# Kernel optimization log

Measured on AMD Instinct MI355X. Metric: run time of the kernel, lower is better.

Reference implementation:

```python
import jax, jax.numpy as jnp
import numpy as np

ROPE_BASE = 10000.0
WINDOW = 1024  # per_layer_sliding_window
SCALE = 0.08838834764831845  # 1/sqrt(128)
NEG_INF = -1e30


def _apply_rope(x, positions):
    # x: [B, S, H, D]; positions: [B, S] int
    D = x.shape[-1]
    inv_freq = 1.0 / (ROPE_BASE ** (jnp.arange(0, D, 2, dtype=jnp.float32) / D))  # [D/2]
    ang = positions.astype(jnp.float32)[..., None] * inv_freq          # [B, S, D/2]
    cos = jnp.cos(ang)[:, :, None, :]                                   # [B, S, 1, D/2]
    sin = jnp.sin(ang)[:, :, None, :]
    x1, x2 = x[..., : D // 2], x[..., D // 2 :]
    return jnp.concatenate([x1 * cos - x2 * sin, x2 * cos + x1 * sin], axis=-1)


def setup_inputs() -> dict:
    key = jax.random.key(0)
    k1, k2, k3, k4 = jax.random.split(key, 4)
    B, S, H, KV, D = 1, 2048, 32, 8, 128
    q = jax.random.normal(k1, (B, S, H, D), dtype=jnp.float32)
    k = jax.random.normal(k2, (B, S, KV, D), dtype=jnp.float32)
    v = jax.random.normal(k3, (B, S, KV, D), dtype=jnp.float32)
    positions = jnp.broadcast_to(jnp.arange(S, dtype=jnp.int32), (B, S))
    sinks = jax.random.normal(k4, (H,), dtype=jnp.float32)
    return {"q": q, "k": k, "v": v, "positions": positions, "sinks": sinks}


def reference(q, k, v, positions, sinks):
    # q: [B,S,H,D]; k,v: [B,S,KV,D]; positions: [B,S]; sinks: [H]
    B, S, H, D = q.shape
    KV = k.shape[2]
    group = H // KV

    qr = _apply_rope(q, positions)
    kr = _apply_rope(k, positions)

    # GQA: expand kv heads to match q heads
    kr = jnp.repeat(kr, group, axis=2)  # [B,S,H,D]
    ve = jnp.repeat(v, group, axis=2)   # [B,S,H,D]

    scores = jnp.einsum("bqhd,bkhd->bhqk", qr, kr) * SCALE  # [B,H,Q,K]

    pq = positions[:, :, None]  # [B,Q,1]
    pk = positions[:, None, :]  # [B,1,K]
    allowed = (pk <= pq) & (pq - pk < WINDOW)               # causal + sliding window
    scores = jnp.where(allowed[:, None, :, :], scores, NEG_INF)

    # softmax with per-head attention sink logit in the denominator
    sink = sinks[None, :, None]                             # [1,H,1]
    m = jnp.maximum(jnp.max(scores, axis=-1), sink)         # [B,H,Q]
    p = jnp.exp(scores - m[..., None])                      # [B,H,Q,K]
    denom = jnp.sum(p, axis=-1) + jnp.exp(sink - m)         # [B,H,Q]
    out = jnp.einsum("bhqk,bkhd->bqhd", p, ve) / denom.transpose(0, 2, 1)[..., None]
    return out  # [B,S,H,D]
```

## Files before the change

### kernel.cpp

```cpp
#include <hip/hip_runtime.h>

#define S_LEN 2048
#define NH 32
#define NKV 8
#define HD 128
#define WINDOW 1024
#define NEG_INF_F -1e30f
#define NEG_L2_10K_O64 -0.2076205059304601f
#define LOG2E_F 1.442695040888963f

typedef unsigned short ushort_t;
typedef __attribute__((ext_vector_type(4))) short bf16x4;
typedef __attribute__((ext_vector_type(8))) short short8;
typedef __attribute__((ext_vector_type(2))) unsigned uint2v;
typedef __attribute__((ext_vector_type(4))) float floatx4;

static __device__ __forceinline__ float fexp2(float x) {
  return __builtin_amdgcn_exp2f(x);
}

static __device__ __forceinline__ ushort_t f2bf(float f) {
  union { float f; unsigned u; } un; un.f = f;
  unsigned r = un.u + 0x7fffu + ((un.u >> 16) & 1u);
  return (ushort_t)(r >> 16);
}

static __device__ __forceinline__ unsigned pack2bf(float a, float b) {
  return (unsigned)f2bf(a) | ((unsigned)f2bf(b) << 16);
}

static __device__ __forceinline__ unsigned packP(float a, float b) {
  unsigned ua = __builtin_bit_cast(unsigned, a) + 0x8000u;
  unsigned ub = __builtin_bit_cast(unsigned, b) + 0x8000u;
  return __builtin_amdgcn_perm(ub, ua, 0x07060302u);
}

__device__ __forceinline__ void gl_lds16(const ushort_t* g, ushort_t* l) {
  __builtin_amdgcn_global_load_lds(
      (const __attribute__((address_space(1))) unsigned int*)g,
      (__attribute__((address_space(3))) unsigned int*)l, 16, 0, 0);
}

__global__ __launch_bounds__(256) void prep_kv(
    const float* __restrict__ k, const float* __restrict__ v,
    const int* __restrict__ positions, ushort_t* __restrict__ Kr,
    ushort_t* __restrict__ Vt) {
  __shared__ float lv[16][129];
  const int kv = blockIdx.x & 7;
  const int s0 = (blockIdx.x >> 3) * 16;
  const int tid = threadIdx.x;
  {
    const int i = tid & 63;
    const int wrow = tid >> 6;
    const float invf = fexp2((float)i * NEG_L2_10K_O64);
#pragma unroll
    for (int it = 0; it < 4; ++it) {
      int s = s0 + it * 4 + wrow;
      float pos = (float)positions[s];
      const float* kp = k + ((size_t)s * NKV + kv) * HD;
      float x1 = kp[i], x2 = kp[i + 64];
      float sn, cs;
      __sincosf(pos * invf, &sn, &cs);
      ushort_t* o = Kr + ((size_t)kv * S_LEN + s) * HD;
      o[i] = f2bf(x1 * cs - x2 * sn);
      o[i + 64] = f2bf(x2 * cs + x1 * sn);
    }
  }
  {
    const int d = tid & 127;
    const int r2 = tid >> 7;
#pragma unroll
    for (int it = 0; it < 8; ++it) {
      int row = it * 2 + r2;
      lv[row][d] = v[((size_t)(s0 + row) * NKV + kv) * HD + d];
    }
  }
  __syncthreads();
  {
    unsigned* Vreg = (unsigned*)(Vt + ((size_t)(kv * 32 + (s0 >> 6)) * HD) * 64);
    const int jg0 = (s0 & 63) >> 1;
#pragma unroll
    for (int it = 0; it < 4; ++it) {
      int idx = it * 256 + tid;
      int d = idx >> 3, jl = idx & 7;
      Vreg[d * 32 + jg0 + jl] = pack2bf(lv[2 * jl][d], lv[2 * jl + 1][d]);
    }
  }
}

__global__ __launch_bounds__(256, 3) void attn_kernel(
    const float* __restrict__ q, const int* __restrict__ positions,
    const float* __restrict__ sinks, const ushort_t* __restrict__ Kr,
    const ushort_t* __restrict__ Vt, float* __restrict__ out) {
  __shared__ __align__(16) ushort_t smem[24576];
  __shared__ float lsx[64];

  const int tid = threadIdx.x;
  const int w = tid >> 6;
  const int lane = tid & 63;
  const int quad = lane >> 4;
  const int l16 = lane & 15;
  const int hp = w >> 1;
  const int kh = w & 1;
  const int kv = blockIdx.x & 7;
  const int bid = blockIdx.x >> 3;
  const int h0 = kv * 4 + hp * 2;
  const float QSCALE = (float)(0.08838834764831845 * 1.4426950408889634);

  const ushort_t* KrH = Kr + (size_t)kv * S_LEN * HD;
  const ushort_t* VtH = Vt + (size_t)kv * 32 * HD * 64;

  int tiles[2];
  int ntiles;
  if (bid < 64) { tiles[0] = bid + 64; tiles[1] = 0; ntiles = 1; }
  else          { tiles[0] = bid - 64; tiles[1] = 127 - bid; ntiles = 2; }

  int kgo0, kgo1, vgo0, vgo1;
  { int key = tid >> 4;          kgo0 = key * HD + (((tid & 15) ^ (key & 15)) * 8); }
  { int s2 = 256 + tid; int key = s2 >> 4;
                                 kgo1 = key * HD + (((s2 & 15) ^ (key & 15)) * 8); }
  { int n = tid;       vgo0 = (n >> 2) * 64 + (((n & 3) ^ ((n >> 4) & 3)) * 8); }
  { int n = 256 + tid; vgo1 = (n >> 2) * 64 + (((n & 3) ^ ((n >> 4) & 3)) * 8); }
  const int kdst0 = (tid & 192) * 8;
  const int kdst1 = (256 + (tid & 192)) * 8;
  const int vdst0 = (tid & 192) * 8;
  const int vdst1 = 2048 + (tid & 192) * 8;
  const int kb8 = kh * 2 + (quad >> 1);
  const int vrd = (l16 * 4 + (kb8 ^ (l16 >> 2))) * 8 + (quad & 1) * 4;
  int kro[4];
#pragma unroll
  for (int t = 0; t < 4; ++t)
    kro[t] = (kh * 16) * 128 + l16 * 128 + (((4 * t + quad) ^ l16) * 8);

  auto stage = [&](int b, int koff) {
    const ushort_t* kb = KrH + (size_t)koff * HD;
    const ushort_t* vb = VtH + (size_t)(koff >> 6) * HD * 64 + (koff & 32);
    ushort_t* Kb = smem + b * 4096;
    ushort_t* Vb = smem + 12288 + b * 4096;
    gl_lds16(kb + kgo0, Kb + kdst0);
    gl_lds16(kb + kgo1, Kb + kdst1);
    gl_lds16(vb + vgo0, Vb + vdst0);
    gl_lds16(vb + vgo1, Vb + vdst1);
  };

  for (int ti = 0; ti < ntiles; ++ti) {
    const int tile = tiles[ti];
    const int q0 = tile * 16;

    {
      const int hw = kv * 4 + w;
      ushort_t* Qsw = smem + w * 2048;
      const float invf = fexp2((float)lane * NEG_L2_10K_O64);
#pragma unroll 4
      for (int row = 0; row < 16; ++row) {
        float pos = (float)positions[q0 + row];
        const float* qp = q + ((size_t)(q0 + row) * NH + hw) * HD;
        float x1 = qp[lane], x2 = qp[lane + 64];
        float sn, cs;
        __sincosf(pos * invf, &sn, &cs);
        float o1 = (x1 * cs - x2 * sn) * QSCALE;
        float o2 = (x2 * cs + x1 * sn) * QSCALE;
        int c1_ = (lane >> 3) ^ row;
        int c2_ = ((lane >> 3) + 8) ^ row;
        Qsw[row * 128 + c1_ * 8 + (lane & 7)] = f2bf(o1);
        Qsw[row * 128 + c2_ * 8 + (lane & 7)] = f2bf(o2);
      }
    }
    __syncthreads();
    short8 qf0[4], qf1[4];
    {
      const ushort_t* Qr0 = smem + (hp * 2) * 2048;
      const ushort_t* Qr1 = smem + (hp * 2 + 1) * 2048;
#pragma unroll
      for (int t = 0; t < 4; ++t) {
        int off = l16 * 128 + (((4 * t + quad) ^ l16) * 8);
        qf0[t] = *(const short8*)&Qr0[off];
        qf1[t] = *(const short8*)&Qr1[off];
      }
    }
    __syncthreads();

    floatx4 OA[8], OB[8];
#pragma unroll
    for (int i = 0; i < 8; ++i) {
      OA[i] = (floatx4){0.f, 0.f, 0.f, 0.f};
      OB[i] = (floatx4){0.f, 0.f, 0.f, 0.f};
    }
    float lsumA = 0.f, lsumB = 0.f;

    const int cbeg = (q0 > 1023) ? ((q0 - 1023) >> 5) : 0;
    const int cend = (q0 + 15) >> 5;

    stage(0, cbeg * 32);
    if (cbeg < cend) stage(1, cbeg * 32 + 32);
    __syncthreads();

    short8 kcur[4];
#pragma unroll
    for (int t = 0; t < 4; ++t) kcur[t] = *(const short8*)&smem[kro[t]];

    int b = 0;
    for (int ci = cbeg; ci <= cend; ++ci) {
      const int koff = ci * 32;
      if (ci + 2 <= cend) {
        int bp2 = (b >= 1) ? (b - 1) : (b + 2);
        stage(bp2, koff + 64);
      }
      const int bn = (b == 2) ? 0 : b + 1;
      short8 knxt[4];
      {
        const ushort_t* KsN = smem + bn * 4096;
#pragma unroll
        for (int t = 0; t < 4; ++t) knxt[t] = *(const short8*)&KsN[kro[t]];
      }

      floatx4 sA = {0.f, 0.f, 0.f, 0.f}, sB = {0.f, 0.f, 0.f, 0.f};
#pragma unroll
      for (int t = 0; t < 4; ++t) {
        sA = __builtin_amdgcn_mfma_f32_16x16x32_bf16(kcur[t], qf0[t], sA, 0, 0, 0);
        sB = __builtin_amdgcn_mfma_f32_16x16x32_bf16(kcur[t], qf1[t], sB, 0, 0, 0);
      }

      if (koff + 31 > q0 || koff < q0 - 1008) {
        const int qp_ = q0 + l16;
        const int kb_ = koff + kh * 16 + quad * 4;
#pragma unroll
        for (int r = 0; r < 4; ++r) {
          int ki = kb_ + r;
          bool ok = (ki <= qp_) && (qp_ - ki < WINDOW);
          if (!ok) { sA[r] = NEG_INF_F; sB[r] = NEG_INF_F; }
        }
      }

      float pA[4], pB[4];
#pragma unroll
      for (int r = 0; r < 4; ++r) { pA[r] = fexp2(sA[r]); pB[r] = fexp2(sB[r]); }
      lsumA += (pA[0] + pA[1]) + (pA[2] + pA[3]);
      lsumB += (pB[0] + pB[1]) + (pB[2] + pB[3]);

      uint2v ua, ub;
      ua[0] = packP(pA[0], pA[1]); ua[1] = packP(pA[2], pA[3]);
      ub[0] = packP(pB[0], pB[1]); ub[1] = packP(pB[2], pB[3]);
      bf16x4 pfA = __builtin_bit_cast(bf16x4, ua);
      bf16x4 pfB = __builtin_bit_cast(bf16x4, ub);

      const ushort_t* VsB = smem + 12288 + b * 4096;
#pragma unroll
      for (int dt = 0; dt < 8; ++dt) {
        bf16x4 vf = *(const bf16x4*)&VsB[vrd + dt * 512];
        OA[dt] = __builtin_amdgcn_mfma_f32_16x16x16bf16_1k(vf, pfA, OA[dt], 0, 0, 0);
        OB[dt] = __builtin_amdgcn_mfma_f32_16x16x16bf16_1k(vf, pfB, OB[dt], 0, 0, 0);
      }

      __syncthreads();
#pragma unroll
      for (int t = 0; t < 4; ++t) kcur[t] = knxt[t];
      b = bn;
    }

    lsumA += __shfl_xor(lsumA, 16); lsumA += __shfl_xor(lsumA, 32);
    lsumB += __shfl_xor(lsumB, 16); lsumB += __shfl_xor(lsumB, 32);
    float* Lf = (float*)smem;
    const int lfb = lane * 4;
    float rlA = 0.f, rlB = 0.f;

    if (kh == 1 && quad == 0) {
      lsx[hp * 32 + l16] = lsumA;
      lsx[hp * 32 + 16 + l16] = lsumB;
    }
#pragma unroll
    for (int m = 0; m < 2; ++m) {
      if (kh == 1) {
#pragma unroll
        for (int t = 0; t < 4; ++t) {
          *(floatx4*)&Lf[((hp * 2 + 0) * 4 + t) * 256 + lfb] = OA[m * 4 + t];
          *(floatx4*)&Lf[((hp * 2 + 1) * 4 + t) * 256 + lfb] = OB[m * 4 + t];
        }
      }
      __syncthreads();
      if (kh == 0) {
        if (m == 0) {
          float denA = lsumA + lsx[hp * 32 + l16] + fexp2(sinks[h0] * LOG2E_F);
          float denB = lsumB + lsx[hp * 32 + 16 + l16] + fexp2(sinks[h0 + 1] * LOG2E_F);
          rlA = 1.0f / denA;
          rlB = 1.0f / denB;
        }
        float* opA = out + ((size_t)(q0 + l16) * NH + h0) * HD + quad * 4;
        float* opB = opA + HD;
#pragma unroll
        for (int t = 0; t < 4; ++t) {
          floatx4 pv = *(const floatx4*)&Lf[((hp * 2 + 0) * 4 + t) * 256 + lfb];
          floatx4 vv;
#pragma unroll
          for (int e = 0; e < 4; ++e) vv[e] = (OA[m * 4 + t][e] + pv[e]) * rlA;
          *(floatx4*)(opA + (m * 4 + t) * 16) = vv;
          pv = *(const floatx4*)&Lf[((hp * 2 + 1) * 4 + t) * 256 + lfb];
#pragma unroll
          for (int e = 0; e < 4; ++e) vv[e] = (OB[m * 4 + t][e] + pv[e]) * rlB;
          *(floatx4*)(opB + (m * 4 + t) * 16) = vv;
        }
      }
      __syncthreads();
    }
  }
}

extern "C" void kernel_launch(void* const* d_in, const int* in_sizes, int n_in,
                              void* d_out, int out_size, void* d_ws, size_t ws_size,
                              hipStream_t stream) {
  const float* q = (const float*)d_in[0];
  const float* k = (const float*)d_in[1];
  const float* v = (const float*)d_in[2];
  const int* positions = (const int*)d_in[3];
  const float* sinks = (const float*)d_in[4];
  float* out = (float*)d_out;

  ushort_t* Kr = (ushort_t*)d_ws;
  ushort_t* Vt = Kr + (size_t)NKV * S_LEN * HD;

  prep_kv<<<NKV * (S_LEN / 16), 256, 0, stream>>>(k, v, positions, Kr, Vt);
  attn_kernel<<<NKV * 96, 256, 0, stream>>>(q, positions, sinks, Kr, Vt, out);
}
```

Before: 132.8 us.

## Per-wave K staging with direct global V fragment loads, drop block barriers

```diff
diff --git a/kernel.cpp b/kernel.cpp
--- a/kernel.cpp
+++ b/kernel.cpp
@@ -77,13 +77,16 @@
   }
   __syncthreads();
   {
-    unsigned* Vreg = (unsigned*)(Vt + ((size_t)(kv * 32 + (s0 >> 6)) * HD) * 64);
+    unsigned* Vreg = (unsigned*)Vt + (size_t)kv * 131072 + (s0 >> 6) * 4096;
     const int jg0 = (s0 & 63) >> 1;
 #pragma unroll
     for (int it = 0; it < 4; ++it) {
       int idx = it * 256 + tid;
       int d = idx >> 3, jl = idx & 7;
-      Vreg[d * 32 + jg0 + jl] = pack2bf(lv[2 * jl][d], lv[2 * jl + 1][d]);
+      int jg = jg0 + jl;
+      int o = (jg >> 3) * 1024 + (d >> 4) * 128 +
+              (((jg >> 1) & 3) * 16 + (d & 15)) * 2 + (jg & 1);
+      Vreg[o] = pack2bf(lv[2 * jl][d], lv[2 * jl + 1][d]);
     }
   }
 }
@@ -92,7 +95,7 @@
     const float* __restrict__ q, const int* __restrict__ positions,
     const float* __restrict__ sinks, const ushort_t* __restrict__ Kr,
     const ushort_t* __restrict__ Vt, float* __restrict__ out) {
-  __shared__ __align__(16) ushort_t smem[24576];
+  __shared__ __align__(16) ushort_t smem[16384];
   __shared__ float lsx[64];
 
   const int tid = threadIdx.x;
@@ -108,39 +111,28 @@
   const float QSCALE = (float)(0.08838834764831845 * 1.4426950408889634);
 
   const ushort_t* KrH = Kr + (size_t)kv * S_LEN * HD;
-  const ushort_t* VtH = Vt + (size_t)kv * 32 * HD * 64;
+  const ushort_t* VtH = Vt + (size_t)kv * 262144;
 
   int tiles[2];
   int ntiles;
   if (bid < 64) { tiles[0] = bid + 64; tiles[1] = 0; ntiles = 1; }
   else          { tiles[0] = bid - 64; tiles[1] = 127 - bid; ntiles = 2; }
 
-  int kgo0, kgo1, vgo0, vgo1;
-  { int key = tid >> 4;          kgo0 = key * HD + (((tid & 15) ^ (key & 15)) * 8); }
-  { int s2 = 256 + tid; int key = s2 >> 4;
-                                 kgo1 = key * HD + (((s2 & 15) ^ (key & 15)) * 8); }
-  { int n = tid;       vgo0 = (n >> 2) * 64 + (((n & 3) ^ ((n >> 4) & 3)) * 8); }
-  { int n = 256 + tid; vgo1 = (n >> 2) * 64 + (((n & 3) ^ ((n >> 4) & 3)) * 8); }
-  const int kdst0 = (tid & 192) * 8;
-  const int kdst1 = (256 + (tid & 192)) * 8;
-  const int vdst0 = (tid & 192) * 8;
-  const int vdst1 = 2048 + (tid & 192) * 8;
-  const int kb8 = kh * 2 + (quad >> 1);
-  const int vrd = (l16 * 4 + (kb8 ^ (l16 >> 2))) * 8 + (quad & 1) * 4;
+  ushort_t* kslot = smem + w * 4096;
+
   int kro[4];
 #pragma unroll
   for (int t = 0; t < 4; ++t)
-    kro[t] = (kh * 16) * 128 + l16 * 128 + (((4 * t + quad) ^ l16) * 8);
-
-  auto stage = [&](int b, int koff) {
-    const ushort_t* kb = KrH + (size_t)koff * HD;
-    const ushort_t* vb = VtH + (size_t)(koff >> 6) * HD * 64 + (koff & 32);
-    ushort_t* Kb = smem + b * 4096;
-    ushort_t* Vb = smem + 12288 + b * 4096;
-    gl_lds16(kb + kgo0, Kb + kdst0);
-    gl_lds16(kb + kgo1, Kb + kdst1);
-    gl_lds16(vb + vgo0, Vb + vdst0);
-    gl_lds16(vb + vgo1, Vb + vdst1);
+    kro[t] = l16 * 128 + (((4 * t + quad) ^ l16) * 8);
+
+  auto wstage = [&](int buf, int koff) {
+    const ushort_t* kb = KrH + (size_t)(koff + kh * 16) * HD;
+    ushort_t* dst = kslot + buf * 2048;
+#pragma unroll
+    for (int i = 0; i < 4; ++i) {
+      int rl = i * 4 + (lane >> 4);
+      gl_lds16(kb + rl * HD + (((lane & 15) ^ rl) * 8), dst + i * 512);
+    }
   };
 
   for (int ti = 0; ti < ntiles; ++ti) {
@@ -191,27 +183,45 @@
     const int cbeg = (q0 > 1023) ? ((q0 - 1023) >> 5) : 0;
     const int cend = (q0 + 15) >> 5;
 
-    stage(0, cbeg * 32);
-    if (cbeg < cend) stage(1, cbeg * 32 + 32);
-    __syncthreads();
-
+    wstage(0, cbeg * 32);
+    if (cbeg < cend) {
+      wstage(1, cbeg * 32 + 32);
+      asm volatile("s_waitcnt vmcnt(4)" ::: "memory");
+    } else {
+      asm volatile("s_waitcnt vmcnt(0)" ::: "memory");
+    }
+    __builtin_amdgcn_sched_barrier(0);
     short8 kcur[4];
 #pragma unroll
-    for (int t = 0; t < 4; ++t) kcur[t] = *(const short8*)&smem[kro[t]];
-
-    int b = 0;
+    for (int t = 0; t < 4; ++t) kcur[t] = *(const short8*)&kslot[kro[t]];
+
     for (int ci = cbeg; ci <= cend; ++ci) {
       const int koff = ci * 32;
+      const int bufc = (ci - cbeg) & 1;
+
+      bf16x4 vf[8];
+      {
+        const ushort_t* vp = VtH + (size_t)(ci * 2 + kh) * 2048 + lane * 4;
+#pragma unroll
+        for (int dt = 0; dt < 8; ++dt) vf[dt] = *(const bf16x4*)(vp + dt * 256);
+      }
+      __builtin_amdgcn_sched_barrier(0);
+
       if (ci + 2 <= cend) {
-        int bp2 = (b >= 1) ? (b - 1) : (b + 2);
-        stage(bp2, koff + 64);
-      }
-      const int bn = (b == 2) ? 0 : b + 1;
+        asm volatile("s_waitcnt lgkmcnt(0)" ::: "memory");
+        __builtin_amdgcn_sched_barrier(0);
+        wstage(bufc, koff + 64);
+        __builtin_amdgcn_sched_barrier(0);
+      }
+
       short8 knxt[4];
-      {
-        const ushort_t* KsN = smem + bn * 4096;
-#pragma unroll
-        for (int t = 0; t < 4; ++t) knxt[t] = *(const short8*)&KsN[kro[t]];
+      if (ci < cend) {
+        if (ci + 2 <= cend) asm volatile("s_waitcnt vmcnt(12)" ::: "memory");
+        else                asm volatile("s_waitcnt vmcnt(8)" ::: "memory");
+        __builtin_amdgcn_sched_barrier(0);
+        const ushort_t* Kn = kslot + (bufc ^ 1) * 2048;
+#pragma unroll
+        for (int t = 0; t < 4; ++t) knxt[t] = *(const short8*)&Kn[kro[t]];
       }
 
       floatx4 sA = {0.f, 0.f, 0.f, 0.f}, sB = {0.f, 0.f, 0.f, 0.f};
@@ -244,19 +254,18 @@
       bf16x4 pfA = __builtin_bit_cast(bf16x4, ua);
       bf16x4 pfB = __builtin_bit_cast(bf16x4, ub);
 
-      const ushort_t* VsB = smem + 12288 + b * 4096;
 #pragma unroll
       for (int dt = 0; dt < 8; ++dt) {
-        bf16x4 vf = *(const bf16x4*)&VsB[vrd + dt * 512];
-        OA[dt] = __builtin_amdgcn_mfma_f32_16x16x16bf16_1k(vf, pfA, OA[dt], 0, 0, 0);
-        OB[dt] = __builtin_amdgcn_mfma_f32_16x16x16bf16_1k(vf, pfB, OB[dt], 0, 0, 0);
-      }
-
-      __syncthreads();
-#pragma unroll
-      for (int t = 0; t < 4; ++t) kcur[t] = knxt[t];
-      b = bn;
-    }
+        OA[dt] = __builtin_amdgcn_mfma_f32_16x16x16bf16_1k(vf[dt], pfA, OA[dt], 0, 0, 0);
+        OB[dt] = __builtin_amdgcn_mfma_f32_16x16x16bf16_1k(vf[dt], pfB, OB[dt], 0, 0, 0);
+      }
+
+      if (ci < cend) {
+#pragma unroll
+        for (int t = 0; t < 4; ++t) kcur[t] = knxt[t];
+      }
+    }
+    __syncthreads();
 
     lsumA += __shfl_xor(lsumA, 16); lsumA += __shfl_xor(lsumA, 32);
     lsumB += __shfl_xor(lsumB, 16); lsumB += __shfl_xor(lsumB, 32);
```

Measured after the change: 374.8 us. 2.82x slower.
